# Optimization experiments

Measured on AMD Instinct MI355X. Metric: run time of the kernel, lower is better.

## Reference

```python
import jax, jax.numpy as jnp
import numpy as np

NUM_HEADS = 12

def setup_inputs() -> dict:
    key = jax.random.key(0)
    k1, k2, k3 = jax.random.split(key, 3)
    B, N, D = 16, 1024, 768
    x = jax.random.normal(k1, (B, N, D), dtype=jnp.float32)
    w_qkv = jax.random.normal(k2, (D, 3 * D), dtype=jnp.float32) * (D ** -0.5)
    b_qkv = jnp.zeros((3 * D,), dtype=jnp.float32)
    w_proj = jax.random.normal(k3, (D, D), dtype=jnp.float32) * (D ** -0.5)
    b_proj = jnp.zeros((D,), dtype=jnp.float32)
    return {"x": x, "w_qkv": w_qkv, "b_qkv": b_qkv, "w_proj": w_proj, "b_proj": b_proj}

def reference(x, w_qkv, b_qkv, w_proj, b_proj):
    B, N, D = x.shape
    H = NUM_HEADS
    Hd = D // H
    scale = Hd ** -0.5
    qkv = x @ w_qkv + b_qkv                       # (B, N, 3D)
    qkv = qkv.reshape(B, N, 3, H, Hd)
    q, k, v = qkv[:, :, 0], qkv[:, :, 1], qkv[:, :, 2]  # (B, N, H, Hd)
    attn = jnp.einsum('bnhd,bmhd->bhnm', q, k) * scale  # (B, H, N, N)
    attn = jax.nn.softmax(attn, axis=-1)
    out = jnp.einsum('bhnm,bmhd->bnhd', attn, v).reshape(B, N, D)
    return out @ w_proj + b_proj
```

## Files before the change

### kernel.cpp

```cpp
#include <hip/hip_runtime.h>


typedef _Float16 half8 __attribute__((ext_vector_type(8)));
typedef _Float16 half4 __attribute__((ext_vector_type(4)));
typedef __fp16   fp16x2 __attribute__((ext_vector_type(2)));
typedef float    f32x4  __attribute__((ext_vector_type(4)));
typedef float    f32x16 __attribute__((ext_vector_type(16)));
typedef unsigned int u32x4 __attribute__((ext_vector_type(4)));

#define DI __device__ __forceinline__

constexpr int   BATCH  = 16;
constexpr int   SEQ    = 1024;
constexpr int   DM     = 768;
constexpr int   NH     = 12;
constexpr int   HD     = 64;
constexpr float SCALE  = 0.125f;
constexpr float LOG2E  = 1.4426950408889634f;

DI void copy16(_Float16* dst, const _Float16* src) {
  *(u32x4*)dst = *(const u32x4*)src;
}

DI int pack_rtz(float a, float b) {
  union { fp16x2 h; int i; } u;
  u.h = __builtin_amdgcn_cvt_pkrtz(a, b);
  return u.i;
}

DI void gld16(const _Float16* g, _Float16* l) {
  __builtin_amdgcn_global_load_lds(
      (const __attribute__((address_space(1))) void*)g,
      (__attribute__((address_space(3))) void*)l, 16, 0, 0);
}

__global__ void cvt_wt2_kernel(const float* __restrict__ wq,
                               _Float16* __restrict__ wqT,
                               const float* __restrict__ wp,
                               _Float16* __restrict__ wpT) {
  __shared__ float tile[32][33];
  const int by = blockIdx.y;
  const float* w; _Float16* wt; int N, nb;
  if (by < 72) { w = wq; wt = wqT; N = 2304; nb = by * 32; }
  else         { w = wp; wt = wpT; N = 768;  nb = (by - 72) * 32; }
  const int K = 768;
  int kb = blockIdx.x * 32;
  int tx = threadIdx.x & 31, ty = threadIdx.x >> 5;
#pragma unroll
  for (int i = 0; i < 32; i += 8)
    tile[ty + i][tx] = w[(size_t)(kb + ty + i) * N + nb + tx];
  __syncthreads();
#pragma unroll
  for (int i = 0; i < 32; i += 8)
    wt[(size_t)(nb + ty + i) * K + kb + tx] = (_Float16)tile[tx][ty + i];
}

__launch_bounds__(256, 3)
__global__ void gemm_qkv_kernel(const float* __restrict__ X,
                                const _Float16* __restrict__ Bt,
                                const float* __restrict__ bias,
                                _Float16* __restrict__ Qo,
                                _Float16* __restrict__ Ko,
                                _Float16* __restrict__ VTo) {
  __shared__ _Float16 sh[16384];
  _Float16* Cs = sh;
  const int tid  = threadIdx.x;
  const int lin  = blockIdx.x;
  const int xcd  = lin & 7, j = lin >> 3;
  const int ct   = j % 18;
  const int m0   = ((j / 18) * 8 + xcd) * 128;
  const int n0   = ct * 128;
  const int w    = tid >> 6, lane = tid & 63;
  const int quad = lane >> 4, l15 = lane & 15;
  const int wr   = w >> 1, wc = w & 1;

  f32x4 acc[4][4] = {};

  const int g0 = tid + w * 64;
  const int r0 = g0 >> 2, s0 = g0 & 3;
  const float*    gaA = X  + (size_t)(m0 + r0) * 768 + s0 * 8;
  const _Float16* gbB = Bt + (size_t)(n0 + r0) * 768 + s0 * 8;
  const int so   = r0 * 32 + s0 * 8;
  const int ldst = w * 1024;

  auto CVT_WRITE = [&](float4 a0, float4 a1, float4 a2, float4 a3,
                       _Float16* As) {
    half8 h0, h1;
    h0[0] = (_Float16)a0.x; h0[1] = (_Float16)a0.y;
    h0[2] = (_Float16)a0.z; h0[3] = (_Float16)a0.w;
    h0[4] = (_Float16)a1.x; h0[5] = (_Float16)a1.y;
    h0[6] = (_Float16)a1.z; h0[7] = (_Float16)a1.w;
    h1[0] = (_Float16)a2.x; h1[1] = (_Float16)a2.y;
    h1[2] = (_Float16)a2.z; h1[3] = (_Float16)a2.w;
    h1[4] = (_Float16)a3.x; h1[5] = (_Float16)a3.y;
    h1[6] = (_Float16)a3.z; h1[7] = (_Float16)a3.w;
    *(half8*)(As + so)       = h0;
    *(half8*)(As + so + 512) = h1;
  };

  {
    float4 a0 = *(const float4*)(gaA);
    float4 a1 = *(const float4*)(gaA + 4);
    float4 a2 = *(const float4*)(gaA + 16 * 768);
    float4 a3 = *(const float4*)(gaA + 16 * 768 + 4);
    CVT_WRITE(a0, a1, a2, a3, sh);
    gld16(gbB,            sh + 4096 + ldst);
    gld16(gbB + 16 * 768, sh + 4096 + ldst + 512);
  }

  for (int kt = 0; kt < 24; ++kt) {
    __syncthreads();
    float4 a0, a1, a2, a3;
    if (kt < 23) {
      const int k0 = (kt + 1) * 32;
      a0 = *(const float4*)(gaA + k0);
      a1 = *(const float4*)(gaA + k0 + 4);
      a2 = *(const float4*)(gaA + k0 + 16 * 768);
      a3 = *(const float4*)(gaA + k0 + 16 * 768 + 4);
      _Float16* Bsn = sh + ((kt + 1) & 1) * 8192 + 4096;
      gld16(gbB + k0,            Bsn + ldst);
      gld16(gbB + k0 + 16 * 768, Bsn + ldst + 512);
    }

    const _Float16* As = sh + (kt & 1) * 8192;
    const _Float16* Bs = As + 4096;

    half8 af[4], bf[4];
#pragma unroll
    for (int mi = 0; mi < 4; mi++)
      af[mi] = *(const half8*)&As[(wr * 64 + mi * 16 + l15) * 32 + quad * 8];
#pragma unroll
    for (int ni = 0; ni < 4; ni++)
      bf[ni] = *(const half8*)&Bs[(wc * 64 + ni * 16 + l15) * 32 + quad * 8];
#pragma unroll
    for (int mi = 0; mi < 4; mi++)
#pragma unroll
      for (int ni = 0; ni < 4; ni++)
        acc[mi][ni] = __builtin_amdgcn_mfma_f32_16x16x32_f16(
            af[mi], bf[ni], acc[mi][ni], 0, 0, 0);

    if (kt < 23)
      CVT_WRITE(a0, a1, a2, a3, sh + ((kt + 1) & 1) * 8192);
  }
  __syncthreads();

  const float oscale = (ct < 6) ? SCALE : 1.0f;
  float bcol[4];
#pragma unroll
  for (int ni = 0; ni < 4; ni++)
    bcol[ni] = bias[n0 + wc * 64 + ni * 16 + l15];

  const int b     = m0 >> 10;
  const int nrow0 = m0 & 1023;
  const int sec   = ct / 6;
  const int h0    = (ct % 6) * 2;

#pragma unroll
  for (int p = 0; p < 2; ++p) {
    if (p) __syncthreads();
    if (wr == p) {
#pragma unroll
      for (int mi = 0; mi < 4; mi++)
#pragma unroll
        for (int ni = 0; ni < 4; ni++) {
          int col = wc * 64 + ni * 16 + l15;
          int row = mi * 16 + quad * 4;
#pragma unroll
          for (int r = 0; r < 4; r++)
            Cs[(row + r) * 136 + col] =
                (_Float16)((acc[mi][ni][r] + bcol[ni]) * oscale);
        }
    }
    __syncthreads();

    if (sec < 2) {
      _Float16* dst = (sec == 0) ? Qo : Ko;
      int row = tid >> 2, seg = tid & 3;
      int hl = seg >> 1, off32 = (seg & 1) * 32;
      _Float16* g = dst +
          ((size_t)((b * NH + h0 + hl) * SEQ + nrow0 + p * 64 + row)) * HD + off32;
      const _Float16* s = &Cs[row * 136 + hl * 64 + off32];
      copy16(g, s);
      copy16(g + 8, s + 8);
      copy16(g + 16, s + 16);
      copy16(g + 24, s + 24);
    } else {
      int c = tid & 127, half = tid >> 7;
      int hl = c >> 6, d = c & 63;
      _Float16 tmp[32];
#pragma unroll
      for (int jj = 0; jj < 32; jj++) tmp[jj] = Cs[(half * 32 + jj) * 136 + c];
      _Float16* g = VTo + ((size_t)((b * NH + h0 + hl) * HD + d)) * SEQ
                        + nrow0 + p * 64 + half * 32;
#pragma unroll
      for (int jj = 0; jj < 4; jj++)
        copy16(g + jj * 8, (const _Float16*)&tmp[jj * 8]);
    }
  }
}

__launch_bounds__(256, 2)
__global__ void attn_kernel(const _Float16* __restrict__ Q,
                            const _Float16* __restrict__ K,
                            const _Float16* __restrict__ VT,
                            _Float16* __restrict__ Oh) {
  __shared__ _Float16 smem[2][2][64 * 72];
  _Float16* OLds = &smem[0][0][0];

  const int tid = threadIdx.x;
  const int i   = blockIdx.x;
  const int bh  = (i & 7) * 24 + ((i >> 3) >> 2);
  const int q0  = ((i >> 3) & 3) * 256;
  const int b   = bh / NH, hh = bh - b * NH;
  const int w   = tid >> 6, lane = tid & 63;
  const int l31 = lane & 31, h = lane >> 5;

  const _Float16* Qg = Q  + (size_t)bh * SEQ * HD;
  const _Float16* Kg = K  + (size_t)bh * SEQ * HD;
  const _Float16* Vg = VT + (size_t)bh * HD * SEQ;

  half8 qb[2][4];
#pragma unroll
  for (int N = 0; N < 2; N++) {
    const _Float16* qrow = Qg + (size_t)(q0 + w * 64 + N * 32 + l31) * HD + h * 8;
#pragma unroll
    for (int s = 0; s < 4; s++)
      qb[N][s] = *(const half8*)(qrow + s * 16);
  }

  const int  sr  = (tid & 127) >> 1;
  const int  sp  = tid & 1;
  const bool isK = tid < 128;
  const _Float16* sg = isK ? (Kg + sr * HD + sp * 32)
                           : (Vg + (size_t)sr * SEQ + sp * 32);
  const int sstep = isK ? 64 * HD : 64;
  const int soff  = (isK ? 0 : 64 * 72) + sr * 72 + sp * 32;

  u32x4 pf[4];
#pragma unroll
  for (int c = 0; c < 4; c++) pf[c] = *(const u32x4*)(sg + c * 8);
#pragma unroll
  for (int c = 0; c < 4; c++) *(u32x4*)(&smem[0][0][0] + soff + c * 8) = pf[c];

  f32x16 of[2][2];
#pragma unroll
  for (int D = 0; D < 2; D++)
#pragma unroll
    for (int N = 0; N < 2; N++)
#pragma unroll
      for (int r = 0; r < 16; r++) of[D][N][r] = 0.f;
  float m_[2] = {-1e30f, -1e30f}, l_[2] = {0.f, 0.f};

  for (int kt = 0; kt < 16; ++kt) {
    if (kt < 15) {
      const _Float16* nsg = sg + (kt + 1) * sstep;
#pragma unroll
      for (int c = 0; c < 4; c++) pf[c] = *(const u32x4*)(nsg + c * 8);
    }
    __syncthreads();
    const _Float16* Ks = &smem[kt & 1][0][0];
    const _Float16* Vs = &smem[kt & 1][1][0];

    f32x16 sf[2][2];
#pragma unroll
    for (int M = 0; M < 2; M++)
#pragma unroll
      for (int N = 0; N < 2; N++)
#pragma unroll
        for (int r = 0; r < 16; r++) sf[M][N][r] = 0.f;
#pragma unroll
    for (int s = 0; s < 4; s++) {
      half8 ka0 = *(const half8*)&Ks[l31 * 72 + s * 16 + h * 8];
      half8 ka1 = *(const half8*)&Ks[(32 + l31) * 72 + s * 16 + h * 8];
#pragma unroll
      for (int N = 0; N < 2; N++) {
        sf[0][N] = __builtin_amdgcn_mfma_f32_32x32x16_f16(ka0, qb[N][s], sf[0][N], 0, 0, 0);
        sf[1][N] = __builtin_amdgcn_mfma_f32_32x32x16_f16(ka1, qb[N][s], sf[1][N], 0, 0, 0);
      }
    }

    float alpha[2], c1[2], tsum[2];
#pragma unroll
    for (int N = 0; N < 2; N++) {
      float tmax = -1e30f;
#pragma unroll
      for (int r = 0; r < 16; r++)
        tmax = fmaxf(tmax, fmaxf(sf[0][N][r], sf[1][N][r]));
      tmax = fmaxf(tmax, __shfl_xor(tmax, 32, 64));
      float mnew = fmaxf(m_[N], tmax);
      alpha[N] = __builtin_amdgcn_exp2f((m_[N] - mnew) * LOG2E);
      m_[N] = mnew;
      c1[N] = mnew * LOG2E;
      tsum[N] = 0.f;
    }

    int pdw[2][2][8];
#pragma unroll
    for (int M = 0; M < 2; M++)
#pragma unroll
      for (int N = 0; N < 2; N++) {
#pragma unroll
        for (int r = 0; r < 16; r++) {
          float p = __builtin_amdgcn_exp2f(sf[M][N][r] * LOG2E - c1[N]);
          sf[M][N][r] = p;
          tsum[N] += p;
        }
#pragma unroll
        for (int u = 0; u < 8; u++)
          pdw[M][N][u] = pack_rtz(sf[M][N][2 * u], sf[M][N][2 * u + 1]);
      }
#pragma unroll
    for (int N = 0; N < 2; N++) {
      tsum[N] += __shfl_xor(tsum[N], 32, 64);
      l_[N] = l_[N] * alpha[N] + tsum[N];
    }
#pragma unroll
    for (int D = 0; D < 2; D++)
#pragma unroll
      for (int N = 0; N < 2; N++)
#pragma unroll
        for (int r = 0; r < 16; r++) of[D][N][r] *= alpha[N];

#pragma unroll
    for (int t = 0; t < 4; ++t) {
      const int M = t >> 1, s2 = (t & 1) * 4;
      half8 va0 = *(const half8*)&Vs[l31 * 72 + t * 16 + h * 8];
      half8 va1 = *(const half8*)&Vs[(32 + l31) * 72 + t * 16 + h * 8];
#pragma unroll
      for (int N = 0; N < 2; N++) {
        int a0 = pdw[M][N][s2 + 0], a1 = pdw[M][N][s2 + 1];
        int a2 = pdw[M][N][s2 + 2], a3 = pdw[M][N][s2 + 3];
        int e0 = h ? a0 : a2, e1 = h ? a1 : a3;
        int r0 = __shfl_xor(e0, 32, 64), r1 = __shfl_xor(e1, 32, 64);
        union { u32x4 u; half8 hv; } bb;
        bb.u[0] = h ? r0 : a0; bb.u[1] = h ? r1 : a1;
        bb.u[2] = h ? a2 : r0; bb.u[3] = h ? a3 : r1;
        of[0][N] = __builtin_amdgcn_mfma_f32_32x32x16_f16(va0, bb.hv, of[0][N], 0, 0, 0);
        of[1][N] = __builtin_amdgcn_mfma_f32_32x32x16_f16(va1, bb.hv, of[1][N], 0, 0, 0);
      }
    }

    if (kt < 15) {
      _Float16* dst = &smem[(kt + 1) & 1][0][0] + soff;
#pragma unroll
      for (int c = 0; c < 4; c++) *(u32x4*)(dst + c * 8) = pf[c];
    }
  }

  __syncthreads();
  float inv[2] = {1.0f / l_[0], 1.0f / l_[1]};
  int* OW = (int*)OLds;
#pragma unroll
  for (int N = 0; N < 2; N++) {
    const int q_local = w * 64 + N * 32 + l31;
#pragma unroll
    for (int D = 0; D < 2; D++)
#pragma unroll
      for (int u = 0; u < 8; u++) {
        int v = pack_rtz(of[D][N][2 * u] * inv[N], of[D][N][2 * u + 1] * inv[N]);
        int dwi = 16 * D + 4 * (u >> 1) + (u & 1) + 2 * h;
        OW[q_local * 36 + dwi] = v;
      }
  }
  __syncthreads();
#pragma unroll
  for (int p = 0; p < 8; p++) {
    int q = p * 32 + (tid >> 3), c = tid & 7;
    *(u32x4*)(Oh + (size_t)(b * SEQ + q0 + q) * DM + hh * HD + c * 8) =
        *(const u32x4*)&OLds[q * 72 + c * 8];
  }
}

__launch_bounds__(256, 3)
__global__ void gemm_proj_kernel(const _Float16* __restrict__ A,
                                 const _Float16* __restrict__ Bt,
                                 const float* __restrict__ bias,
                                 float* __restrict__ out) {
  __shared__ _Float16 sh[16384];
  const int tid  = threadIdx.x;
  const int lin  = blockIdx.x;
  const int xcd  = lin & 7, j = lin >> 3;
  const int ct   = j % 6;
  const int m0   = ((j / 6) * 8 + xcd) * 128;
  const int n0   = ct * 128;
  const int w    = tid >> 6, lane = tid & 63;
  const int quad = lane >> 4, l15 = lane & 15;
  const int wr   = w >> 1, wc = w & 1;

  f32x4 acc[4][4] = {};

  const int g0 = tid + w * 64;
  const int r0 = g0 >> 2, s0 = g0 & 3;
  const _Float16* gaA = A  + (size_t)(m0 + r0) * 768 + s0 * 8;
  const _Float16* gaB = Bt + (size_t)(n0 + r0) * 768 + s0 * 8;
  const int ldst = w * 1024;

  auto STAGE = [&](int buf, int kt) {
    _Float16* As = sh + buf * 8192;
    _Float16* Bs = As + 4096;
    const _Float16* a = gaA + kt * 32;
    const _Float16* b = gaB + kt * 32;
    gld16(a,            As + ldst);
    gld16(a + 16 * 768, As + ldst + 512);
    gld16(b,            Bs + ldst);
    gld16(b + 16 * 768, Bs + ldst + 512);
  };

  STAGE(0, 0);

  for (int kt = 0; kt < 24; ++kt) {
    __syncthreads();
    if (kt < 23) STAGE((kt + 1) & 1, kt + 1);

    const _Float16* As = sh + (kt & 1) * 8192;
    const _Float16* Bs = As + 4096;

    half8 af[4], bf[4];
#pragma unroll
    for (int mi = 0; mi < 4; mi++)
      af[mi] = *(const half8*)&As[(wr * 64 + mi * 16 + l15) * 32 + quad * 8];
#pragma unroll
    for (int ni = 0; ni < 4; ni++)
      bf[ni] = *(const half8*)&Bs[(wc * 64 + ni * 16 + l15) * 32 + quad * 8];
#pragma unroll
    for (int mi = 0; mi < 4; mi++)
#pragma unroll
      for (int ni = 0; ni < 4; ni++)
        acc[mi][ni] = __builtin_amdgcn_mfma_f32_16x16x32_f16(
            af[mi], bf[ni], acc[mi][ni], 0, 0, 0);
  }

  float bcol[4];
#pragma unroll
  for (int ni = 0; ni < 4; ni++)
    bcol[ni] = bias[n0 + wc * 64 + ni * 16 + l15];
#pragma unroll
  for (int mi = 0; mi < 4; mi++)
#pragma unroll
    for (int ni = 0; ni < 4; ni++) {
      int col = n0 + wc * 64 + ni * 16 + l15;
      int row = m0 + wr * 64 + mi * 16 + quad * 4;
#pragma unroll
      for (int r = 0; r < 4; r++)
        out[(size_t)(row + r) * 768 + col] = acc[mi][ni][r] + bcol[ni];
    }
}

extern "C" void kernel_launch(void* const* d_in, const int* in_sizes, int n_in,
                              void* d_out, int out_size, void* d_ws, size_t ws_size,
                              hipStream_t stream) {
  const float* x      = (const float*)d_in[0];
  const float* w_qkv  = (const float*)d_in[1];
  const float* b_qkv  = (const float*)d_in[2];
  const float* w_proj = (const float*)d_in[3];
  const float* b_proj = (const float*)d_in[4];
  float* out = (float*)d_out;

  char* ws = (char*)d_ws;
  _Float16* wqkvT  = (_Float16*)(ws);
  _Float16* wprojT = (_Float16*)(ws + 3538944);
  _Float16* Qp     = (_Float16*)(ws + 4718592);
  _Float16* Kp     = (_Float16*)(ws + 29884416);
  _Float16* VTp    = (_Float16*)(ws + 55050240);
  _Float16* Ohp    = (_Float16*)(ws + 80216064);

  cvt_wt2_kernel<<<dim3(24, 96), 256, 0, stream>>>(w_qkv, wqkvT, w_proj, wprojT);
  gemm_qkv_kernel<<<dim3(2304), 256, 0, stream>>>(x, wqkvT, b_qkv, Qp, Kp, VTp);
  attn_kernel<<<dim3(768), 256, 0, stream>>>(Qp, Kp, VTp, Ohp);
  gemm_proj_kernel<<<dim3(768), 256, 0, stream>>>(Ohp, wprojT, b_proj, out);
}
```

Measured before the change: 303.0 us.

## Load A fragments directly into registers and swizzle B LDS layout

Both GEMM kernels now load the A operand straight from global memory into the MFMA fragment registers, with one-tile-ahead register prefetch, instead of staging it through shared memory. Only B stays double-buffered in LDS, which halves the LDS footprint. An XOR swizzle is applied to the B global-to-LDS mapping and to the fragment reads to reduce bank conflicts. In exchange, the two waves in each row pair each load the same A rows from global memory, using more global/L2 bandwidth and more registers for the prefetched fp32 data.

```diff
diff --git a/kernel.cpp b/kernel.cpp
--- a/kernel.cpp
+++ b/kernel.cpp
@@ -62,7 +62,7 @@
                                 _Float16* __restrict__ Qo,
                                 _Float16* __restrict__ Ko,
                                 _Float16* __restrict__ VTo) {
-  __shared__ _Float16 sh[16384];
+  __shared__ _Float16 sh[8704];
   _Float16* Cs = sh;
   const int tid  = threadIdx.x;
   const int lin  = blockIdx.x;
@@ -76,71 +76,62 @@
 
   f32x4 acc[4][4] = {};
 
-  const int g0 = tid + w * 64;
-  const int r0 = g0 >> 2, s0 = g0 & 3;
-  const float*    gaA = X  + (size_t)(m0 + r0) * 768 + s0 * 8;
-  const _Float16* gbB = Bt + (size_t)(n0 + r0) * 768 + s0 * 8;
-  const int so   = r0 * 32 + s0 * 8;
+  const int r0  = (w * 128 + lane) >> 2;
+  const int s0x = ((lane & 3) ^ (2 * ((lane >> 5) & 1)));
+  const _Float16* gbB = Bt + (size_t)(n0 + r0) * 768 + s0x * 8;
   const int ldst = w * 1024;
 
-  auto CVT_WRITE = [&](float4 a0, float4 a1, float4 a2, float4 a3,
-                       _Float16* As) {
-    half8 h0, h1;
-    h0[0] = (_Float16)a0.x; h0[1] = (_Float16)a0.y;
-    h0[2] = (_Float16)a0.z; h0[3] = (_Float16)a0.w;
-    h0[4] = (_Float16)a1.x; h0[5] = (_Float16)a1.y;
-    h0[6] = (_Float16)a1.z; h0[7] = (_Float16)a1.w;
-    h1[0] = (_Float16)a2.x; h1[1] = (_Float16)a2.y;
-    h1[2] = (_Float16)a2.z; h1[3] = (_Float16)a2.w;
-    h1[4] = (_Float16)a3.x; h1[5] = (_Float16)a3.y;
-    h1[6] = (_Float16)a3.z; h1[7] = (_Float16)a3.w;
-    *(half8*)(As + so)       = h0;
-    *(half8*)(As + so + 512) = h1;
-  };
-
-  {
-    float4 a0 = *(const float4*)(gaA);
-    float4 a1 = *(const float4*)(gaA + 4);
-    float4 a2 = *(const float4*)(gaA + 16 * 768);
-    float4 a3 = *(const float4*)(gaA + 16 * 768 + 4);
-    CVT_WRITE(a0, a1, a2, a3, sh);
-    gld16(gbB,            sh + 4096 + ldst);
-    gld16(gbB + 16 * 768, sh + 4096 + ldst + 512);
-  }
+  const float* gA = X + (size_t)(m0 + wr * 64 + l15) * 768 + quad * 8;
+
+  float4 pa0[4], pa1[4];
+#pragma unroll
+  for (int mi = 0; mi < 4; mi++) {
+    pa0[mi] = *(const float4*)(gA + mi * 12288);
+    pa1[mi] = *(const float4*)(gA + mi * 12288 + 4);
+  }
+  gld16(gbB,            sh + ldst);
+  gld16(gbB + 16 * 768, sh + ldst + 512);
+
+  const int qa = (quad ^ (2 * ((l15 >> 3) & 1))) * 8;
 
   for (int kt = 0; kt < 24; ++kt) {
     __syncthreads();
-    float4 a0, a1, a2, a3;
+
+    half8 af[4];
+#pragma unroll
+    for (int mi = 0; mi < 4; mi++) {
+      half8 h;
+      h[0] = (_Float16)pa0[mi].x; h[1] = (_Float16)pa0[mi].y;
+      h[2] = (_Float16)pa0[mi].z; h[3] = (_Float16)pa0[mi].w;
+      h[4] = (_Float16)pa1[mi].x; h[5] = (_Float16)pa1[mi].y;
+      h[6] = (_Float16)pa1[mi].z; h[7] = (_Float16)pa1[mi].w;
+      af[mi] = h;
+    }
+
     if (kt < 23) {
       const int k0 = (kt + 1) * 32;
-      a0 = *(const float4*)(gaA + k0);
-      a1 = *(const float4*)(gaA + k0 + 4);
-      a2 = *(const float4*)(gaA + k0 + 16 * 768);
-      a3 = *(const float4*)(gaA + k0 + 16 * 768 + 4);
-      _Float16* Bsn = sh + ((kt + 1) & 1) * 8192 + 4096;
+#pragma unroll
+      for (int mi = 0; mi < 4; mi++) {
+        pa0[mi] = *(const float4*)(gA + k0 + mi * 12288);
+        pa1[mi] = *(const float4*)(gA + k0 + mi * 12288 + 4);
+      }
+      _Float16* Bsn = sh + ((kt + 1) & 1) * 4096;
       gld16(gbB + k0,            Bsn + ldst);
       gld16(gbB + k0 + 16 * 768, Bsn + ldst + 512);
     }
 
-    const _Float16* As = sh + (kt & 1) * 8192;
-    const _Float16* Bs = As + 4096;
-
-    half8 af[4], bf[4];
-#pragma unroll
-    for (int mi = 0; mi < 4; mi++)
-      af[mi] = *(const half8*)&As[(wr * 64 + mi * 16 + l15) * 32 + quad * 8];
+    const _Float16* Bs = sh + (kt & 1) * 4096;
+    half8 bf[4];
 #pragma unroll
     for (int ni = 0; ni < 4; ni++)
-      bf[ni] = *(const half8*)&Bs[(wc * 64 + ni * 16 + l15) * 32 + quad * 8];
+      bf[ni] = *(const half8*)&Bs[(wc * 64 + ni * 16 + l15) * 32 + qa];
+
 #pragma unroll
     for (int mi = 0; mi < 4; mi++)
 #pragma unroll
       for (int ni = 0; ni < 4; ni++)
         acc[mi][ni] = __builtin_amdgcn_mfma_f32_16x16x32_f16(
             af[mi], bf[ni], acc[mi][ni], 0, 0, 0);
-
-    if (kt < 23)
-      CVT_WRITE(a0, a1, a2, a3, sh + ((kt + 1) & 1) * 8192);
   }
   __syncthreads();
 
@@ -376,7 +367,7 @@
                                  const _Float16* __restrict__ Bt,
                                  const float* __restrict__ bias,
                                  float* __restrict__ out) {
-  __shared__ _Float16 sh[16384];
+  __shared__ _Float16 sh[8192];
   const int tid  = threadIdx.x;
   const int lin  = blockIdx.x;
   const int xcd  = lin & 7, j = lin >> 3;
@@ -389,39 +380,45 @@
 
   f32x4 acc[4][4] = {};
 
-  const int g0 = tid + w * 64;
-  const int r0 = g0 >> 2, s0 = g0 & 3;
-  const _Float16* gaA = A  + (size_t)(m0 + r0) * 768 + s0 * 8;
-  const _Float16* gaB = Bt + (size_t)(n0 + r0) * 768 + s0 * 8;
+  const int r0  = (w * 128 + lane) >> 2;
+  const int s0x = ((lane & 3) ^ (2 * ((lane >> 5) & 1)));
+  const _Float16* gbB = Bt + (size_t)(n0 + r0) * 768 + s0x * 8;
   const int ldst = w * 1024;
 
-  auto STAGE = [&](int buf, int kt) {
-    _Float16* As = sh + buf * 8192;
-    _Float16* Bs = As + 4096;
-    const _Float16* a = gaA + kt * 32;
-    const _Float16* b = gaB + kt * 32;
-    gld16(a,            As + ldst);
-    gld16(a + 16 * 768, As + ldst + 512);
-    gld16(b,            Bs + ldst);
-    gld16(b + 16 * 768, Bs + ldst + 512);
-  };
-
-  STAGE(0, 0);
+  const _Float16* gA = A + (size_t)(m0 + wr * 64 + l15) * 768 + quad * 8;
+
+  half8 pa[4];
+#pragma unroll
+  for (int mi = 0; mi < 4; mi++)
+    pa[mi] = *(const half8*)(gA + mi * 12288);
+  gld16(gbB,            sh + ldst);
+  gld16(gbB + 16 * 768, sh + ldst + 512);
+
+  const int qa = (quad ^ (2 * ((l15 >> 3) & 1))) * 8;
 
   for (int kt = 0; kt < 24; ++kt) {
     __syncthreads();
-    if (kt < 23) STAGE((kt + 1) & 1, kt + 1);
-
-    const _Float16* As = sh + (kt & 1) * 8192;
-    const _Float16* Bs = As + 4096;
-
-    half8 af[4], bf[4];
-#pragma unroll
-    for (int mi = 0; mi < 4; mi++)
-      af[mi] = *(const half8*)&As[(wr * 64 + mi * 16 + l15) * 32 + quad * 8];
+
+    half8 af[4];
+#pragma unroll
+    for (int mi = 0; mi < 4; mi++) af[mi] = pa[mi];
+
+    if (kt < 23) {
+      const int k0 = (kt + 1) * 32;
+#pragma unroll
+      for (int mi = 0; mi < 4; mi++)
+        pa[mi] = *(const half8*)(gA + k0 + mi * 12288);
+      _Float16* Bsn = sh + ((kt + 1) & 1) * 4096;
+      gld16(gbB + k0,            Bsn + ldst);
+      gld16(gbB + k0 + 16 * 768, Bsn + ldst + 512);
+    }
+
+    const _Float16* Bs = sh + (kt & 1) * 4096;
+    half8 bf[4];
 #pragma unroll
     for (int ni = 0; ni < 4; ni++)
-      bf[ni] = *(const half8*)&Bs[(wc * 64 + ni * 16 + l15) * 32 + quad * 8];
+      bf[ni] = *(const half8*)&Bs[(wc * 64 + ni * 16 + l15) * 32 + qa];
+
 #pragma unroll
     for (int mi = 0; mi < 4; mi++)
 #pragma unroll
```

Result: slower. 463.7 us (+53.0%).
